# Optimization experiments

Measured on AMD Instinct MI355X. Metric: run time of the kernel, lower is better.

## Reference

```python
import jax, jax.numpy as jnp
import numpy as np

B, C, H, W = 4, 512, 96, 96
NH = 8
HD = C // NH
NC = 128
D = 768
L = H * W
EPS = 1e-5  # torch LayerNorm default


def _l2n(x, axis):
    # F.normalize: x / max(||x||, 1e-12)
    return x / jnp.maximum(jnp.linalg.norm(x, axis=axis, keepdims=True), 1e-12)


def _ln2d(x, g, b):
    # LayerNorm2d: normalize over channel dim of (B,C,H,W)
    mu = x.mean(1, keepdims=True)
    var = ((x - mu) ** 2).mean(1, keepdims=True)
    return (x - mu) / jnp.sqrt(var + EPS) * g[None, :, None, None] + b[None, :, None, None]


def _conv1x1(x, w):
    return jnp.einsum('oc,bchw->bohw', w, x)


def setup_inputs() -> dict:
    key = jax.random.key(0)
    ks = jax.random.split(key, 9)
    s = 0.02
    return {
        'img_feats': jax.random.normal(ks[0], (B, C, H, W), jnp.float32),
        'cls_embs': jax.random.normal(ks[1], (NC, D), jnp.float32),
        'cls_logits': jax.random.normal(ks[2], (B, NC), jnp.float32),
        'seg_logits': jax.random.normal(ks[3], (B, 1, H, W), jnp.float32),
        'gamma_g': jnp.ones((D,), jnp.float32), 'beta_g': jnp.zeros((D,), jnp.float32),
        'gamma_f': jnp.ones((C,), jnp.float32), 'beta_f': jnp.zeros((C,), jnp.float32),
        'attn_scale': jnp.ones((NH, 1, 1), jnp.float32),
        'Wg': jax.random.normal(ks[4], (C, D), jnp.float32) * s,
        'Wqkv': jax.random.normal(ks[5], (3 * C, C), jnp.float32) * s,
        'Wo': jax.random.normal(ks[6], (C, C), jnp.float32) * s,
        'bo': jnp.zeros((C,), jnp.float32),
        'gamma_n': jnp.ones((C,), jnp.float32), 'beta_n': jnp.zeros((C,), jnp.float32),
        'W1': jax.random.normal(ks[7], (C, C), jnp.float32) * s, 'b1': jnp.zeros((C,), jnp.float32),
        'W2': jax.random.normal(ks[8], (C, C), jnp.float32) * s, 'b2': jnp.zeros((C,), jnp.float32),
    }


def reference(img_feats, cls_embs, cls_logits, seg_logits, gamma_g, beta_g,
              gamma_f, beta_f, attn_scale, Wg, Wqkv, Wo, bo, gamma_n, beta_n,
              W1, b1, W2, b2):
    xn = _ln2d(img_feats, gamma_f, beta_f)
    # guide LayerNorm over embedding dim
    mu = cls_embs.mean(-1, keepdims=True)
    var = ((cls_embs - mu) ** 2).mean(-1, keepdims=True)
    cn = (cls_embs - mu) / jnp.sqrt(var + EPS) * gamma_g + beta_g
    g = (cn @ Wg.T).reshape(NC, NH, HD)  # nc nh hd

    qkv = _conv1x1(xn, Wqkv).reshape(B, 3, NH, HD, L)
    q, k, v = qkv[:, 0], qkv[:, 1], qkv[:, 2]  # each (B,NH,HD,L)

    # cosine guide map + min-max normalization + softmax-weighted aggregation over classes
    gm = jnp.einsum('nhd,bhdl->bhnl', _l2n(g, -1), _l2n(q, -2))
    gm = gm - gm.min(-1, keepdims=True)
    gm = gm / gm.max(-1, keepdims=True)
    gm = (jax.nn.softmax(gm, axis=2) * gm).sum(2, keepdims=True)  # (B,NH,1,L)

    # auxiliary guide map from cls logits + masked pooling of k
    cls_obj = jnp.einsum('nhd,bn->bhd', g, cls_logits)
    mask = jax.nn.sigmoid(seg_logits)  # (B,1,H,W)
    seg_obj = (mask * k.reshape(B, C, H, W)).sum((2, 3)) / mask.sum((2, 3))  # (B,C)
    obj = _l2n(cls_obj + seg_obj.reshape(B, NH, HD), -1)
    aux = jnp.einsum('bhd,bhdl->bhl', obj, _l2n(k, -2))[:, :, None, :]
    aux = aux - aux.min(-1, keepdims=True)
    aux = aux / aux.max(-1, keepdims=True)
    gm = gm * aux

    v = gm * v
    # channel (transposed) cosine attention: (B,NH,HD,HD)
    attn = jnp.einsum('bhdl,bhel->bhde', _l2n(q, -1), _l2n(k, -1)) * attn_scale
    out = jnp.einsum('bhde,bhel->bhdl', jax.nn.softmax(attn, -1), v).reshape(B, C, H, W)

    x = img_feats + _conv1x1(out, Wo) + bo[None, :, None, None]
    # ConvMlp with pre-norm: LayerNorm2d -> 1x1 conv -> GELU -> 1x1 conv
    fin = _ln2d(x, gamma_n, beta_n)
    h = jax.nn.gelu(_conv1x1(fin, W1) + b1[None, :, None, None], approximate=False)
    return x + _conv1x1(h, W2) + b2[None, :, None, None]
```

## Files before the change

kernel.cpp:

```cpp
#include <hip/hip_runtime.h>
#include <hip/hip_bf16.h>
#include <math.h>

#define BB 4
#define CC 512
#define NHEAD 8
#define HDIM 64
#define NCLS 128
#define DD 768
#define LL 9216
#define BLPIX 36864
#define EPSV 1e-5f
#define GMBLK 144
#define AUXBLK 36
#define LSPLIT 8
#define NLT 72

typedef __hip_bfloat16 bf16;
typedef __attribute__((ext_vector_type(8))) short short8v;
typedef __attribute__((ext_vector_type(4))) short short4v;
typedef __attribute__((ext_vector_type(4))) float f32x4;

__device__ __forceinline__ float bf2f(bf16 v){ return __bfloat162float(v); }
__device__ __forceinline__ bf16 f2bf(float v){ return __float2bfloat16(v); }
__device__ __forceinline__ short bfbits(float v){ bf16 b = __float2bfloat16(v); return *reinterpret_cast<short*>(&b); }
__device__ __forceinline__ float s2f(short s){ bf16 b = *reinterpret_cast<bf16*>(&s); return __bfloat162float(b); }

__global__ __launch_bounds__(256) void fuse_ln_k(const float* __restrict__ X,
    const float* __restrict__ lng, const float* __restrict__ lnb,
    bf16* __restrict__ xnT){
  __shared__ float sred[2][4][64];
  __shared__ float muS[64], rsS[64];
  __shared__ float t[64][65];
  int p0 = blockIdx.x * 64;
  int b = p0 / LL, l0 = p0 - b * LL;
  int tid = threadIdx.x;
  int cg = tid >> 6, l = tid & 63;
  const float* base = X + (size_t)b * CC * LL + l0 + l;
  float s = 0.f, ss = 0.f;
  for (int c = cg * 128; c < cg * 128 + 128; c++){
    float v = base[(size_t)c * LL];
    s += v; ss += v * v;
  }
  sred[0][cg][l] = s; sred[1][cg][l] = ss;
  __syncthreads();
  if (tid < 64){
    float st = sred[0][0][tid] + sred[0][1][tid] + sred[0][2][tid] + sred[0][3][tid];
    float sst = sred[1][0][tid] + sred[1][1][tid] + sred[1][2][tid] + sred[1][3][tid];
    float m = st * (1.0f / CC);
    float var = sst * (1.0f / CC) - m * m;
    muS[tid] = m; rsS[tid] = rsqrtf(var + EPSV);
  }
  __syncthreads();
  int pr = tid >> 4;
  int cc = (tid & 15) * 4;
  for (int cb = 0; cb < 8; cb++){
    int c0 = cb * 64;
    #pragma unroll
    for (int i = 0; i < 16; i++){
      int idx = i * 256 + tid;
      int cl = idx >> 6, ll2 = idx & 63;
      t[cl][ll2] = X[(size_t)b * CC * LL + (size_t)(c0 + cl) * LL + l0 + ll2];
    }
    __syncthreads();
    #pragma unroll
    for (int i = 0; i < 4; i++){
      int pl = pr + i * 16;
      int p = p0 + pl;
      float m = muS[pl], r = rsS[pl];
      short4v pk;
      #pragma unroll
      for (int e = 0; e < 4; e++){
        int c = c0 + cc + e;
        pk[e] = bfbits((t[cc + e][pl] - m) * r * lng[c] + lnb[c]);
      }
      *(short4v*)&xnT[(size_t)p * CC + c0 + cc] = pk;
    }
    __syncthreads();
  }
}

__global__ void wcast_k(const float* __restrict__ wqkv, const float* __restrict__ wo,
                        const float* __restrict__ w1, const float* __restrict__ w2,
                        bf16* __restrict__ oq, bf16* __restrict__ oo,
                        bf16* __restrict__ o1, bf16* __restrict__ o2){
  int i = blockIdx.x * 256 + threadIdx.x;
  int e = i * 4;
  const float* src; bf16* dst; int off;
  if (e < 786432){ src = wqkv; dst = oq; off = e; }
  else if (e < 1048576){ src = wo; dst = oo; off = e - 786432; }
  else if (e < 1310720){ src = w1; dst = o1; off = e - 1048576; }
  else { src = w2; dst = o2; off = e - 1310720; }
  float4 v = *reinterpret_cast<const float4*>(src + off);
  short4v pk;
  pk[0] = bfbits(v.x); pk[1] = bfbits(v.y); pk[2] = bfbits(v.z); pk[3] = bfbits(v.w);
  *(short4v*)&dst[off] = pk;
}

__global__ void statsred_k(const float2* __restrict__ statp, float* __restrict__ mu, float* __restrict__ rs){
  int p = blockIdx.x * 256 + threadIdx.x;
  if (p >= BLPIX) return;
  float s = 0.f, ss = 0.f;
  #pragma unroll
  for (int part = 0; part < 4; part++){
    float2 v = statp[part * BLPIX + p];
    s += v.x; ss += v.y;
  }
  float m = s * (1.0f / CC);
  float var = ss * (1.0f / CC) - m * m;
  mu[p] = m; rs[p] = rsqrtf(var + EPSV);
}

__global__ void rownorm_red_k(const float* __restrict__ qssp, const float* __restrict__ kssp,
                              float* __restrict__ qn, float* __restrict__ kn){
  int row = blockIdx.x;
  const float* src = (row < 2048) ? qssp : kssp;
  int r = (row < 2048) ? row : row - 2048;
  float s = 0.f;
  for (int i = threadIdx.x; i < NLT; i += 64) s += src[(size_t)r * NLT + i];
  #pragma unroll
  for (int m = 1; m < 64; m <<= 1) s += __shfl_xor(s, m);
  if (threadIdx.x == 0){
    float nv = fmaxf(sqrtf(s), 1e-12f);
    if (row < 2048) qn[r] = nv; else kn[r] = nv;
  }
}

template<int MODE>
__global__ __launch_bounds__(256, 2) void mgemm_k(
    const bf16* __restrict__ A,
    const bf16* __restrict__ B,
    const float* __restrict__ residf,
    const bf16* __restrict__ residb,
    const float* __restrict__ bias,
    const float* __restrict__ mu, const float* __restrict__ rs,
    const float* __restrict__ lng, const float* __restrict__ lnb,
    float2* __restrict__ statp,
    float* __restrict__ qssp, float* __restrict__ kssp,
    bf16* __restrict__ qo, bf16* __restrict__ ko, bf16* __restrict__ vo,
    bf16* __restrict__ xT_out,
    float* __restrict__ xo,
    bf16* __restrict__ ho)
{
  __shared__ short Asm[128 * 64];
  __shared__ short Bsm[128 * 64];
  __shared__ float sredf[512];
  int tid = threadIdx.x;
  int lane = tid & 63, wv = tid >> 6;
  int wr = wv >> 1, wc = wv & 1;
  int r15 = lane & 15, g = lane >> 4, h7 = lane & 7;
  int gx = gridDim.x;
  int flat = blockIdx.y * gx + blockIdx.x;
  int cpx = (gx * gridDim.y) >> 3;
  int swz = (flat & 7) * cpx + (flat >> 3);
  int m0 = (swz % gx) * 128, n0 = (swz / gx) * 128;
  int srow = tid >> 3, skkg = tid & 7;
  int sslot = ((skkg ^ (srow & 7))) * 8;

  f32x4 acc[4][4];
  #pragma unroll
  for (int i = 0; i < 4; i++)
    #pragma unroll
    for (int j = 0; j < 4; j++) acc[i][j] = (f32x4){0.f, 0.f, 0.f, 0.f};

  short8v pa[4], pb[4];
  auto loadAB = [&](int it){
    int k0 = it * 64;
    if (MODE == 2){
      int c0 = k0 + skkg * 8;
      float ga[8], be[8];
      *(float4*)&ga[0] = *(const float4*)&lng[c0];
      *(float4*)&ga[4] = *(const float4*)&lng[c0 + 4];
      *(float4*)&be[0] = *(const float4*)&lnb[c0];
      *(float4*)&be[4] = *(const float4*)&lnb[c0 + 4];
      #pragma unroll
      for (int r = 0; r < 4; r++){
        pa[r] = *reinterpret_cast<const short8v*>(A + (size_t)(m0 + r * 32 + srow) * 512 + c0);
        int rp = n0 + r * 32 + srow;
        float mm = mu[rp], rr = rs[rp];
        short8v raw = *reinterpret_cast<const short8v*>(B + (size_t)rp * 512 + c0);
        short8v ov;
        #pragma unroll
        for (int e = 0; e < 8; e++){
          float v = (s2f(raw[e]) - mm) * rr * ga[e] + be[e];
          ov[e] = bfbits(v);
        }
        pb[r] = ov;
      }
    } else {
      #pragma unroll
      for (int r = 0; r < 4; r++){
        pa[r] = *reinterpret_cast<const short8v*>(A + (size_t)(m0 + r * 32 + srow) * 512 + k0 + skkg * 8);
        pb[r] = *reinterpret_cast<const short8v*>(B + (size_t)(n0 + r * 32 + srow) * 512 + k0 + skkg * 8);
      }
    }
  };

  loadAB(0);
  for (int it = 0; it < 8; ++it){
    __syncthreads();
    #pragma unroll
    for (int r = 0; r < 4; r++){
      int row = r * 32 + srow;
      *(short8v*)&Asm[row * 64 + sslot] = pa[r];
      *(short8v*)&Bsm[row * 64 + sslot] = pb[r];
    }
    __syncthreads();
    if (it < 7) loadAB(it + 1);
    #pragma unroll
    for (int s = 0; s < 2; s++){
      int slot = ((s * 4 + g) ^ h7) * 8;
      short8v af[4], bf_[4];
      #pragma unroll
      for (int i = 0; i < 4; i++){
        af[i]  = *(const short8v*)&Asm[(wr * 64 + i * 16 + r15) * 64 + slot];
        bf_[i] = *(const short8v*)&Bsm[(wc * 64 + i * 16 + r15) * 64 + slot];
      }
      #pragma unroll
      for (int i = 0; i < 4; i++)
        #pragma unroll
        for (int j = 0; j < 4; j++){
          if (MODE == 2)
            acc[i][j] = __builtin_amdgcn_mfma_f32_16x16x32_bf16(bf_[i], af[j], acc[i][j], 0, 0, 0);
          else
            acc[i][j] = __builtin_amdgcn_mfma_f32_16x16x32_bf16(af[i], bf_[j], acc[i][j], 0, 0, 0);
        }
    }
  }

  int bIdx = n0 / LL;
  int lbase = n0 - bIdx * LL;
  if (MODE == 0){
    int part = m0 >> 9;
    if (part < 2){
      bf16* dst = (part == 0) ? qo : ko;
      int chb = (m0 & 511) + wr * 64;
      #pragma unroll
      for (int i = 0; i < 4; i++)
        #pragma unroll
        for (int j = 0; j < 4; j++){
          int l = lbase + wc * 64 + j * 16 + r15;
          #pragma unroll
          for (int e = 0; e < 4; e++){
            int ch = chb + i * 16 + g * 4 + e;
            dst[(size_t)bIdx * CC * LL + (size_t)ch * LL + l] = f2bf(acc[i][j][e]);
          }
        }
      #pragma unroll
      for (int i = 0; i < 4; i++)
        #pragma unroll
        for (int e = 0; e < 4; e++){
          float ssv = acc[i][0][e]*acc[i][0][e] + acc[i][1][e]*acc[i][1][e]
                    + acc[i][2][e]*acc[i][2][e] + acc[i][3][e]*acc[i][3][e];
          #pragma unroll
          for (int msk = 1; msk < 16; msk <<= 1) ssv += __shfl_xor(ssv, msk);
          if (r15 == 0) sredf[wv * 64 + i * 16 + g * 4 + e] = ssv;
        }
      __syncthreads();
      if (tid < 128){
        int wrr = tid >> 6, chL = tid & 63;
        float tot = sredf[(wrr * 2) * 64 + chL] + sredf[(wrr * 2 + 1) * 64 + chL];
        int c = (m0 & 511) + wrr * 64 + chL;
        int row = bIdx * 512 + c;
        int ltile = lbase >> 7;
        float* dd = (part == 0) ? qssp : kssp;
        dd[(size_t)row * NLT + ltile] = tot;
      }
    } else {
      int chb = (m0 & 511) + wr * 64;
      #pragma unroll
      for (int i = 0; i < 4; i++)
        #pragma unroll
        for (int j = 0; j < 4; j++){
          int l = lbase + wc * 64 + j * 16 + r15;
          int ch = chb + i * 16 + g * 4;
          short4v pk;
          #pragma unroll
          for (int e = 0; e < 4; e++) pk[e] = bfbits(acc[i][j][e]);
          *(short4v*)&vo[((size_t)bIdx * LL + l) * CC + ch] = pk;
        }
    }
  } else if (MODE == 1){
    float sj[4] = {0.f,0.f,0.f,0.f}, ssj[4] = {0.f,0.f,0.f,0.f};
    #pragma unroll
    for (int i = 0; i < 4; i++)
      #pragma unroll
      for (int j = 0; j < 4; j++){
        int l = lbase + wc * 64 + j * 16 + r15;
        int chm = m0 + wr * 64 + i * 16 + g * 4;
        short4v pk;
        #pragma unroll
        for (int e = 0; e < 4; e++){
          int m = chm + e;
          size_t o = (size_t)bIdx * CC * LL + (size_t)m * LL + l;
          float xv = residf[o] + acc[i][j][e] + bias[m];
          pk[e] = bfbits(xv);
          sj[j] += xv; ssj[j] += xv * xv;
        }
        *(short4v*)&xT_out[((size_t)bIdx * LL + l) * CC + chm] = pk;
      }
    #pragma unroll
    for (int j = 0; j < 4; j++){
      sj[j] += __shfl_xor(sj[j], 16); sj[j] += __shfl_xor(sj[j], 32);
      ssj[j] += __shfl_xor(ssj[j], 16); ssj[j] += __shfl_xor(ssj[j], 32);
    }
    if (g == 0){
      #pragma unroll
      for (int j = 0; j < 4; j++){
        sredf[wv * 128 + j * 32 + r15 * 2 + 0] = sj[j];
        sredf[wv * 128 + j * 32 + r15 * 2 + 1] = ssj[j];
      }
    }
    __syncthreads();
    if (tid < 128){
      int wv2 = tid >> 6, lane2 = tid & 63, j2 = lane2 >> 4, r2 = lane2 & 15;
      float s   = sredf[wv2 * 128 + j2 * 32 + r2 * 2 + 0] + sredf[(wv2 + 2) * 128 + j2 * 32 + r2 * 2 + 0];
      float ss2 = sredf[wv2 * 128 + j2 * 32 + r2 * 2 + 1] + sredf[(wv2 + 2) * 128 + j2 * 32 + r2 * 2 + 1];
      int p = n0 + wv2 * 64 + j2 * 16 + r2;
      statp[(m0 >> 7) * BLPIX + p] = make_float2(s, ss2);
    }
  } else if (MODE == 3){
    #pragma unroll
    for (int i = 0; i < 4; i++)
      #pragma unroll
      for (int j = 0; j < 4; j++){
        int l = lbase + wc * 64 + j * 16 + r15;
        int chm = m0 + wr * 64 + i * 16 + g * 4;
        short4v rv = *(const short4v*)&residb[((size_t)bIdx * LL + l) * CC + chm];
        #pragma unroll
        for (int e = 0; e < 4; e++){
          int m = chm + e;
          size_t o = (size_t)bIdx * CC * LL + (size_t)m * LL + l;
          xo[o] = s2f(rv[e]) + acc[i][j][e] + bias[m];
        }
      }
  } else {
    #pragma unroll
    for (int i = 0; i < 4; i++)
      #pragma unroll
      for (int j = 0; j < 4; j++){
        int mm = m0 + wr * 64 + j * 16 + r15;
        float bv = bias[mm];
        #pragma unroll
        for (int e = 0; e < 4; e++){
          int n = n0 + wc * 64 + i * 16 + g * 4 + e;
          float t = acc[i][j][e] + bv;
          float gv = 0.5f * t * (1.0f + erff(t * 0.70710678118654752f));
          ho[(size_t)n * CC + mm] = f2bf(gv);
        }
      }
  }
}

__global__ void clsg_k(const float* __restrict__ cls_embs, const float* __restrict__ gamma_g,
                       const float* __restrict__ beta_g, const float* __restrict__ Wg,
                       float* __restrict__ g, bf16* __restrict__ gnb){
  __shared__ float cn[DD];
  __shared__ float red[256];
  __shared__ float gsh[CC];
  __shared__ float nrm[NHEAD];
  int n = blockIdx.x;
  const float* e = cls_embs + (size_t)n * DD;
  float s = 0.f, ss = 0.f;
  for (int i = threadIdx.x; i < DD; i += 256){ float v = e[i]; s += v; ss += v * v; }
  red[threadIdx.x] = s; __syncthreads();
  for (int st = 128; st > 0; st >>= 1){ if (threadIdx.x < st) red[threadIdx.x] += red[threadIdx.x + st]; __syncthreads(); }
  float mean = red[0] / DD; __syncthreads();
  red[threadIdx.x] = ss; __syncthreads();
  for (int st = 128; st > 0; st >>= 1){ if (threadIdx.x < st) red[threadIdx.x] += red[threadIdx.x + st]; __syncthreads(); }
  float var = red[0] / DD - mean * mean;
  float rstd = rsqrtf(var + EPSV);
  __syncthreads();
  for (int i = threadIdx.x; i < DD; i += 256) cn[i] = (e[i] - mean) * rstd * gamma_g[i] + beta_g[i];
  __syncthreads();
  for (int c = threadIdx.x; c < CC; c += 256){
    const float* w = Wg + (size_t)c * DD;
    float a = 0.f;
    #pragma unroll 8
    for (int d = 0; d < DD; d++) a += cn[d] * w[d];
    gsh[c] = a;
  }
  __syncthreads();
  if (threadIdx.x < NHEAD){
    float a = 0.f;
    for (int d = 0; d < HDIM; d++){ float v = gsh[threadIdx.x * HDIM + d]; a += v * v; }
    nrm[threadIdx.x] = fmaxf(sqrtf(a), 1e-12f);
  }
  __syncthreads();
  for (int c = threadIdx.x; c < CC; c += 256){
    g[(size_t)n * CC + c] = gsh[c];
    gnb[(size_t)n * CC + c] = f2bf(gsh[c] / nrm[c >> 6]);
  }
}

__global__ void clsobj_k(const float* __restrict__ g, const float* __restrict__ cls_l,
                         float* __restrict__ cls_obj){
  int idx = blockIdx.x * 256 + threadIdx.x;
  if (idx >= BB * CC) return;
  int b = idx >> 9, c = idx & 511;
  float a = 0.f;
  for (int n = 0; n < NCLS; n++) a += g[(size_t)n * CC + c] * cls_l[b * NCLS + n];
  cls_obj[idx] = a;
}

__global__ __launch_bounds__(256) void gm1_k(const bf16* __restrict__ q, const bf16* __restrict__ gnb,
        float* __restrict__ pmin, float* __restrict__ pmax){
  __shared__ bf16 qs[64 * 68];
  __shared__ float sspart[4][64];
  __shared__ float rq[64];
  int bh = blockIdx.x, lt = blockIdx.y;
  int l0 = lt * 64;
  int t = threadIdx.x;
  int b = bh >> 3, h = bh & 7;
  int w = t >> 6, lane = t & 63, r15 = lane & 15, g = lane >> 4;
  const bf16* qp = q + (size_t)b * CC * LL + (size_t)h * HDIM * LL + l0;
  #pragma unroll
  for (int i2 = 0; i2 < 4; i2++){
    int idx = t + i2 * 256;
    int d = idx >> 4, lch = (idx & 15) * 4;
    short4v vv = *reinterpret_cast<const short4v*>(qp + (size_t)d * LL + lch);
    *(short4v*)&qs[d * 68 + lch] = vv;
  }
  __syncthreads();
  {
    int l = t & 63, dg = t >> 6;
    float ss = 0.f;
    #pragma unroll
    for (int dd = 0; dd < 16; dd++){ float v = bf2f(qs[(dg * 16 + dd) * 68 + l]); ss += v * v; }
    sspart[dg][l] = ss;
  }
  __syncthreads();
  if (t < 64){
    float ss = sspart[0][t] + sspart[1][t] + sspart[2][t] + sspart[3][t];
    rq[t] = 1.0f / fmaxf(sqrtf(ss), 1e-12f);
  }
  __syncthreads();
  short8v ag[2][2];
  #pragma unroll
  for (int i = 0; i < 2; i++)
    #pragma unroll
    for (int kt = 0; kt < 2; kt++)
      ag[i][kt] = *reinterpret_cast<const short8v*>(gnb + (size_t)(w * 32 + i * 16 + r15) * CC + h * 64 + kt * 32 + g * 8);
  short8v bq[4][2];
  #pragma unroll
  for (int j = 0; j < 4; j++){
    float rqv = rq[j * 16 + r15];
    #pragma unroll
    for (int kt = 0; kt < 2; kt++){
      short8v bb;
      #pragma unroll
      for (int jj = 0; jj < 8; jj++){
        int d = kt * 32 + g * 8 + jj;
        bb[jj] = bfbits(bf2f(qs[d * 68 + j * 16 + r15]) * rqv);
      }
      bq[j][kt] = bb;
    }
  }
  f32x4 acc[2][4];
  #pragma unroll
  for (int i = 0; i < 2; i++)
    #pragma unroll
    for (int j = 0; j < 4; j++) acc[i][j] = (f32x4){0.f,0.f,0.f,0.f};
  #pragma unroll
  for (int kt = 0; kt < 2; kt++)
    #pragma unroll
    for (int i = 0; i < 2; i++)
      #pragma unroll
      for (int j = 0; j < 4; j++)
        acc[i][j] = __builtin_amdgcn_mfma_f32_16x16x32_bf16(ag[i][kt], bq[j][kt], acc[i][j], 0, 0, 0);
  #pragma unroll
  for (int i = 0; i < 2; i++)
    #pragma unroll
    for (int e = 0; e < 4; e++){
      float mn = acc[i][0][e], mx = acc[i][0][e];
      #pragma unroll
      for (int j = 1; j < 4; j++){ mn = fminf(mn, acc[i][j][e]); mx = fmaxf(mx, acc[i][j][e]); }
      #pragma unroll
      for (int msk = 1; msk < 16; msk <<= 1){
        mn = fminf(mn, __shfl_xor(mn, msk));
        mx = fmaxf(mx, __shfl_xor(mx, msk));
      }
      if (r15 == 0){
        int n = w * 32 + i * 16 + g * 4 + e;
        pmin[((size_t)bh * 128 + n) * GMBLK + lt] = mn;
        pmax[((size_t)bh * 128 + n) * GMBLK + lt] = mx;
      }
    }
}

__global__ void gmred_k(const float* __restrict__ pmin, const float* __restrict__ pmax,
                        float* __restrict__ gmin, float* __restrict__ gms){
  __shared__ float rmn[64], rmx[64];
  int row = blockIdx.x;
  float mn = 1e30f, mx = -1e30f;
  for (int i = threadIdx.x; i < GMBLK; i += 64){
    mn = fminf(mn, pmin[(size_t)row * GMBLK + i]);
    mx = fmaxf(mx, pmax[(size_t)row * GMBLK + i]);
  }
  rmn[threadIdx.x] = mn; rmx[threadIdx.x] = mx; __syncthreads();
  for (int st = 32; st > 0; st >>= 1){
    if (threadIdx.x < st){
      rmn[threadIdx.x] = fminf(rmn[threadIdx.x], rmn[threadIdx.x + st]);
      rmx[threadIdx.x] = fmaxf(rmx[threadIdx.x], rmx[threadIdx.x + st]);
    }
    __syncthreads();
  }
  if (threadIdx.x == 0){ gmin[row] = rmn[0]; gms[row] = rmx[0] - rmn[0]; }
}

__global__ void seg_k(const float* __restrict__ seg, const bf16* __restrict__ k, float* __restrict__ seg_num){
  __shared__ float red[256];
  int bc = blockIdx.x;
  int b = bc >> 9;
  const bf16* p = k + (size_t)bc * LL;
  const float* sp = seg + (size_t)b * LL;
  float s = 0.f;
  for (int i = threadIdx.x; i < LL; i += 256){
    float m = 1.0f / (1.0f + expf(-sp[i]));
    s += m * bf2f(p[i]);
  }
  red[threadIdx.x] = s; __syncthreads();
  for (int st = 128; st > 0; st >>= 1){ if (threadIdx.x < st) red[threadIdx.x] += red[threadIdx.x + st]; __syncthreads(); }
  if (threadIdx.x == 0) seg_num[bc] = red[0];
}

__global__ void segden_k(const float* __restrict__ seg, float* __restrict__ den){
  __shared__ float red[256];
  int b = blockIdx.x;
  const float* sp = seg + (size_t)b * LL;
  float s = 0.f;
  for (int i = threadIdx.x; i < LL; i += 256) s += 1.0f / (1.0f + expf(-sp[i]));
  red[threadIdx.x] = s; __syncthreads();
  for (int st = 128; st > 0; st >>= 1){ if (threadIdx.x < st) red[threadIdx.x] += red[threadIdx.x + st]; __syncthreads(); }
  if (threadIdx.x == 0) den[b] = red[0];
}

__global__ void obj_k(const float* __restrict__ cls_obj, const float* __restrict__ seg_num,
                      const float* __restrict__ den, float* __restrict__ obj){
  __shared__ float sval[2048];
  __shared__ float nrm[32];
  int tid = threadIdx.x;
  #pragma unroll
  for (int i = 0; i < 8; i++){
    int idx = tid + i * 256;
    int b = idx >> 9;
    sval[idx] = cls_obj[idx] + seg_num[idx] / den[b];
  }
  __syncthreads();
  if (tid < 32){
    float s = 0.f;
    for (int d = 0; d < 64; d++){ float v = sval[tid * 64 + d]; s += v * v; }
    nrm[tid] = fmaxf(sqrtf(s), 1e-12f);
  }
  __syncthreads();
  #pragma unroll
  for (int i = 0; i < 8; i++){
    int idx = tid + i * 256;
    obj[idx] = sval[idx] / nrm[idx >> 6];
  }
}

__global__ void aux_k(const bf16* __restrict__ k, const float* __restrict__ obj, float* __restrict__ aux,
                      float* __restrict__ pmin, float* __restrict__ pmax){
  __shared__ float os[64];
  __shared__ float rmn[256], rmx[256];
  int bh = blockIdx.x, lt = blockIdx.y;
  int b = bh >> 3, h = bh & 7;
  int l = lt * 256 + threadIdx.x;
  if (threadIdx.x < 64) os[threadIdx.x] = obj[bh * 64 + threadIdx.x];
  __syncthreads();
  const bf16* kp = k + (size_t)b * CC * LL + (size_t)h * HDIM * LL + l;
  float ss = 0.f, dot = 0.f;
  #pragma unroll 8
  for (int d = 0; d < 64; d++){ float v = bf2f(kp[(size_t)d * LL]); ss += v * v; dot += os[d] * v; }
  float av = dot / fmaxf(sqrtf(ss), 1e-12f);
  aux[(size_t)bh * LL + l] = av;
  rmn[threadIdx.x] = av; rmx[threadIdx.x] = av; __syncthreads();
  for (int st = 128; st > 0; st >>= 1){
    if (threadIdx.x < st){
      rmn[threadIdx.x] = fminf(rmn[threadIdx.x], rmn[threadIdx.x + st]);
      rmx[threadIdx.x] = fmaxf(rmx[threadIdx.x], rmx[threadIdx.x + st]);
    }
    __syncthreads();
  }
  if (threadIdx.x == 0){ pmin[bh * AUXBLK + lt] = rmn[0]; pmax[bh * AUXBLK + lt] = rmx[0]; }
}

__global__ void auxred_k(const float* __restrict__ pmin, const float* __restrict__ pmax,
                         float* __restrict__ amin, float* __restrict__ ams){
  __shared__ float rmn[64], rmx[64];
  int bh = blockIdx.x;
  float mn = 1e30f, mx = -1e30f;
  for (int i = threadIdx.x; i < AUXBLK; i += 64){
    mn = fminf(mn, pmin[bh * AUXBLK + i]);
    mx = fmaxf(mx, pmax[bh * AUXBLK + i]);
  }
  rmn[threadIdx.x] = mn; rmx[threadIdx.x] = mx; __syncthreads();
  for (int st = 32; st > 0; st >>= 1){
    if (threadIdx.x < st){
      rmn[threadIdx.x] = fminf(rmn[threadIdx.x], rmn[threadIdx.x + st]);
      rmx[threadIdx.x] = fmaxf(rmx[threadIdx.x], rmx[threadIdx.x + st]);
    }
    __syncthreads();
  }
  if (threadIdx.x == 0){ amin[bh] = rmn[0]; ams[bh] = rmx[0] - rmn[0]; }
}

__global__ __launch_bounds__(256) void attn_k(const bf16* __restrict__ q, const bf16* __restrict__ k,
                                              float* __restrict__ part){
  __shared__ float red[4 * 4096];
  int ls = blockIdx.x, bh = blockIdx.y;
  int b = bh >> 3, h = bh & 7;
  int t = threadIdx.x;
  int w = t >> 6, lane = t & 63, r15 = lane & 15, g = lane >> 4;
  const bf16* qp = q + (size_t)b * CC * LL + (size_t)h * HDIM * LL;
  const bf16* kp = k + (size_t)b * CC * LL + (size_t)h * HDIM * LL;
  int kbase = ls * 1152 + w * 288;
  f32x4 acc[4][4];
  #pragma unroll
  for (int i = 0; i < 4; i++)
    #pragma unroll
    for (int j = 0; j < 4; j++) acc[i][j] = (f32x4){0.f,0.f,0.f,0.f};
  for (int ks = 0; ks < 9; ks++){
    int koff = kbase + ks * 32 + g * 8;
    short8v aq[4], bk[4];
    #pragma unroll
    for (int i = 0; i < 4; i++) aq[i] = *reinterpret_cast<const short8v*>(qp + (size_t)(i * 16 + r15) * LL + koff);
    #pragma unroll
    for (int j = 0; j < 4; j++) bk[j] = *reinterpret_cast<const short8v*>(kp + (size_t)(j * 16 + r15) * LL + koff);
    #pragma unroll
    for (int i = 0; i < 4; i++)
      #pragma unroll
      for (int j = 0; j < 4; j++)
        acc[i][j] = __builtin_amdgcn_mfma_f32_16x16x32_bf16(aq[i], bk[j], acc[i][j], 0, 0, 0);
  }
  #pragma unroll
  for (int i = 0; i < 4; i++)
    #pragma unroll
    for (int j = 0; j < 4; j++)
      #pragma unroll
      for (int e = 0; e < 4; e++)
        red[w * 4096 + (i * 16 + g * 4 + e) * 64 + j * 16 + r15] = acc[i][j][e];
  __syncthreads();
  #pragma unroll
  for (int it = 0; it < 16; it++){
    int idx = t + it * 256;
    part[((size_t)(bh * LSPLIT + ls)) * 4096 + idx] = red[idx] + red[4096 + idx] + red[8192 + idx] + red[12288 + idx];
  }
}

__global__ void smax_k(const float* __restrict__ part, const float* __restrict__ qn,
                       const float* __restrict__ kn, const float* __restrict__ scale,
                       bf16* __restrict__ Pb){
  __shared__ float As[64 * 65];
  int bh = blockIdx.x;
  int h = bh & 7;
  int tid = threadIdx.x;
  #pragma unroll
  for (int i = 0; i < 16; i++){
    int cell = tid + i * 256;
    int d = cell >> 6, e = cell & 63;
    float s = 0.f;
    #pragma unroll
    for (int ls = 0; ls < LSPLIT; ls++) s += part[((size_t)(bh * LSPLIT + ls)) * 4096 + cell];
    As[d * 65 + e] = s * scale[h] / (qn[bh * 64 + d] * kn[bh * 64 + e]);
  }
  __syncthreads();
  if (tid < 64){
    int d = tid;
    float mx = -1e30f;
    for (int e = 0; e < 64; e++) mx = fmaxf(mx, As[d * 65 + e]);
    float sum = 0.f;
    for (int e = 0; e < 64; e++){ float ev = expf(As[d * 65 + e] - mx); As[d * 65 + e] = ev; sum += ev; }
    float inv = 1.0f / sum;
    for (int e = 0; e < 64; e++) Pb[(size_t)bh * 4096 + d * 64 + e] = f2bf(As[d * 65 + e] * inv);
  }
}

__global__ __launch_bounds__(256) void pv_k(const bf16* __restrict__ q, const bf16* __restrict__ gnb,
      const float* __restrict__ aux,
      const float* __restrict__ gmin, const float* __restrict__ gms,
      const float* __restrict__ amin, const float* __restrict__ ams,
      const bf16* __restrict__ Pb, const bf16* __restrict__ vT, bf16* __restrict__ outT){
  __shared__ bf16 qs[64 * 68];
  __shared__ float sspart[4][64];
  __shared__ float rq[64];
  __shared__ float gminS[128], rgmsS[128];
  __shared__ float separt[4][64], setpart[4][64];
  __shared__ float wl[64];
  int bh = blockIdx.x, lt = blockIdx.y;
  int l0 = lt * 64;
  int t = threadIdx.x;
  int b = bh >> 3, h = bh & 7;
  int w = t >> 6, lane = t & 63, r15 = lane & 15, g = lane >> 4;
  if (t < 128){ gminS[t] = gmin[bh * 128 + t]; rgmsS[t] = 1.0f / gms[bh * 128 + t]; }
  const bf16* qp = q + (size_t)b * CC * LL + (size_t)h * HDIM * LL + l0;
  #pragma unroll
  for (int i2 = 0; i2 < 4; i2++){
    int idx = t + i2 * 256;
    int d = idx >> 4, lch = (idx & 15) * 4;
    short4v vv = *reinterpret_cast<const short4v*>(qp + (size_t)d * LL + lch);
    *(short4v*)&qs[d * 68 + lch] = vv;
  }
  __syncthreads();
  {
    int l = t & 63, dg = t >> 6;
    float ss = 0.f;
    #pragma unroll
    for (int dd = 0; dd < 16; dd++){ float v = bf2f(qs[(dg * 16 + dd) * 68 + l]); ss += v * v; }
    sspart[dg][l] = ss;
  }
  __syncthreads();
  if (t < 64){
    float ss = sspart[0][t] + sspart[1][t] + sspart[2][t] + sspart[3][t];
    rq[t] = 1.0f / fmaxf(sqrtf(ss), 1e-12f);
  }
  __syncthreads();
  short8v ag[2][2];
  #pragma unroll
  for (int i = 0; i < 2; i++)
    #pragma unroll
    for (int kt = 0; kt < 2; kt++)
      ag[i][kt] = *reinterpret_cast<const short8v*>(gnb + (size_t)(w * 32 + i * 16 + r15) * CC + h * 64 + kt * 32 + g * 8);
  short8v bq[4][2];
  #pragma unroll
  for (int j = 0; j < 4; j++){
    float rqv = rq[j * 16 + r15];
    #pragma unroll
    for (int kt = 0; kt < 2; kt++){
      short8v bb;
      #pragma unroll
      for (int jj = 0; jj < 8; jj++){
        int d = kt * 32 + g * 8 + jj;
        bb[jj] = bfbits(bf2f(qs[d * 68 + j * 16 + r15]) * rqv);
      }
      bq[j][kt] = bb;
    }
  }
  f32x4 acc[2][4];
  #pragma unroll
  for (int i = 0; i < 2; i++)
    #pragma unroll
    for (int j = 0; j < 4; j++) acc[i][j] = (f32x4){0.f,0.f,0.f,0.f};
  #pragma unroll
  for (int kt = 0; kt < 2; kt++)
    #pragma unroll
    for (int i = 0; i < 2; i++)
      #pragma unroll
      for (int j = 0; j < 4; j++)
        acc[i][j] = __builtin_amdgcn_mfma_f32_16x16x32_bf16(ag[i][kt], bq[j][kt], acc[i][j], 0, 0, 0);
  float seL[4] = {0.f,0.f,0.f,0.f}, setL[4] = {0.f,0.f,0.f,0.f};
  #pragma unroll
  for (int i = 0; i < 2; i++)
    #pragma unroll
    for (int j = 0; j < 4; j++)
      #pragma unroll
      for (int e = 0; e < 4; e++){
        int n = w * 32 + i * 16 + g * 4 + e;
        float tt = (acc[i][j][e] - gminS[n]) * rgmsS[n];
        float ee = __expf(tt);
        seL[j] += ee; setL[j] += ee * tt;
      }
  #pragma unroll
  for (int j = 0; j < 4; j++){
    seL[j] += __shfl_xor(seL[j], 16); seL[j] += __shfl_xor(seL[j], 32);
    setL[j] += __shfl_xor(setL[j], 16); setL[j] += __shfl_xor(setL[j], 32);
  }
  if (g == 0){
    #pragma unroll
    for (int j = 0; j < 4; j++){ separt[w][j * 16 + r15] = seL[j]; setpart[w][j * 16 + r15] = setL[j]; }
  }
  __syncthreads();
  if (t < 64){
    float se = separt[0][t] + separt[1][t] + separt[2][t] + separt[3][t];
    float st = setpart[0][t] + setpart[1][t] + setpart[2][t] + setpart[3][t];
    float gmred = st / se;
    float auxn = (aux[(size_t)bh * LL + l0 + t] - amin[bh]) / ams[bh];
    wl[t] = gmred * auxn;
  }
  __syncthreads();
  short8v ap[4][2];
  #pragma unroll
  for (int i = 0; i < 4; i++)
    #pragma unroll
    for (int kt = 0; kt < 2; kt++)
      ap[i][kt] = *reinterpret_cast<const short8v*>(Pb + (size_t)bh * 4096 + (i * 16 + r15) * 64 + kt * 32 + g * 8);
  const bf16* vrow = vT + ((size_t)b * LL + l0 + w * 16 + r15) * CC + h * 64;
  short8v bv[2];
  #pragma unroll
  for (int kt = 0; kt < 2; kt++) bv[kt] = *reinterpret_cast<const short8v*>(vrow + kt * 32 + g * 8);
  f32x4 oacc[4];
  #pragma unroll
  for (int i = 0; i < 4; i++) oacc[i] = (f32x4){0.f,0.f,0.f,0.f};
  #pragma unroll
  for (int kt = 0; kt < 2; kt++)
    #pragma unroll
    for (int i = 0; i < 4; i++)
      oacc[i] = __builtin_amdgcn_mfma_f32_16x16x32_bf16(ap[i][kt], bv[kt], oacc[i], 0, 0, 0);
  float wlv = wl[w * 16 + r15];
  bf16* orow = outT + ((size_t)b * LL + l0 + w * 16 + r15) * CC + h * 64;
  #pragma unroll
  for (int i = 0; i < 4; i++){
    short4v pk;
    #pragma unroll
    for (int e = 0; e < 4; e++) pk[e] = bfbits(oacc[i][e] * wlv);
    *(short4v*)&orow[i * 16 + g * 4] = pk;
  }
}

extern "C" void kernel_launch(void* const* d_in, const int* in_sizes, int n_in,
                              void* d_out, int out_size, void* d_ws, size_t ws_size,
                              hipStream_t stream){
  const float* img        = (const float*)d_in[0];
  const float* cls_embs   = (const float*)d_in[1];
  const float* cls_logits = (const float*)d_in[2];
  const float* seg        = (const float*)d_in[3];
  const float* gamma_g    = (const float*)d_in[4];
  const float* beta_g     = (const float*)d_in[5];
  const float* gamma_f    = (const float*)d_in[6];
  const float* beta_f     = (const float*)d_in[7];
  const float* attn_scale = (const float*)d_in[8];
  const float* Wg         = (const float*)d_in[9];
  const float* Wqkv       = (const float*)d_in[10];
  const float* Wo         = (const float*)d_in[11];
  const float* bo         = (const float*)d_in[12];
  const float* gamma_n    = (const float*)d_in[13];
  const float* beta_n     = (const float*)d_in[14];
  const float* W1         = (const float*)d_in[15];
  const float* b1         = (const float*)d_in[16];
  const float* W2         = (const float*)d_in[17];
  const float* b2         = (const float*)d_in[18];
  float* outp = (float*)d_out;
  (void)in_sizes; (void)n_in; (void)out_size;

  char* wsb = (char*)d_ws;
  size_t off = 0;
  auto alloc = [&](size_t bytes)->char*{
    char* p = wsb + off;
    off += (bytes + 255) & ~(size_t)255;
    return p;
  };
  float* mu1   = (float*)alloc((size_t)BLPIX * 4);
  float* rs1   = (float*)alloc((size_t)BLPIX * 4);
  float2* statp= (float2*)alloc((size_t)4 * BLPIX * 8);
  float* qssp  = (float*)alloc((size_t)2048 * NLT * 4);
  float* kssp  = (float*)alloc((size_t)2048 * NLT * 4);
  float* qn    = (float*)alloc(2048 * 4);
  float* kn    = (float*)alloc(2048 * 4);
  float* gbuf  = (float*)alloc((size_t)NCLS * CC * 4);
  bf16*  gnbb  = (bf16*)alloc((size_t)NCLS * CC * 2);
  float* clsov = (float*)alloc(2048 * 4);
  float* segn  = (float*)alloc(2048 * 4);
  float* segd  = (float*)alloc(256);
  float* objv  = (float*)alloc(2048 * 4);
  float* gminp = (float*)alloc((size_t)32 * 128 * GMBLK * 4);
  float* gmaxp = (float*)alloc((size_t)32 * 128 * GMBLK * 4);
  float* gminv = (float*)alloc(4096 * 4);
  float* gmsv  = (float*)alloc(4096 * 4);
  float* auxv  = (float*)alloc((size_t)32 * LL * 4);
  float* apmin = (float*)alloc(32 * AUXBLK * 4);
  float* apmax = (float*)alloc(32 * AUXBLK * 4);
  float* aminv = (float*)alloc(256);
  float* amsv  = (float*)alloc(256);
  bf16*  Pb    = (bf16*)alloc((size_t)32 * 4096 * 2);
  float* apart = (float*)alloc((size_t)32 * LSPLIT * 4096 * 4);
  bf16* qb    = (bf16*)alloc((size_t)BB * CC * LL * 2);
  bf16* kb    = (bf16*)alloc((size_t)BB * CC * LL * 2);
  bf16* wqkvb = (bf16*)alloc((size_t)1536 * 512 * 2);
  bf16* wob   = (bf16*)alloc((size_t)512 * 512 * 2);
  bf16* w1b   = (bf16*)alloc((size_t)512 * 512 * 2);
  bf16* w2b   = (bf16*)alloc((size_t)512 * 512 * 2);
  bf16* vT  = (bf16*)d_out;
  bf16* xnT = (bf16*)((char*)d_out + (size_t)BB * CC * LL * 2);
  bf16* outT = kb;
  bf16* xT   = qb;
  bf16* hbT  = kb;
  if (off > ws_size) return;

  wcast_k<<<1536, 256, 0, stream>>>(Wqkv, Wo, W1, W2, wqkvb, wob, w1b, w2b);
  fuse_ln_k<<<576, 256, 0, stream>>>(img, gamma_f, beta_f, xnT);
  mgemm_k<0><<<dim3(12, 288), 256, 0, stream>>>(wqkvb, xnT, nullptr, nullptr, nullptr,
      nullptr, nullptr, nullptr, nullptr, nullptr, qssp, kssp,
      qb, kb, vT, nullptr, nullptr, nullptr);
  rownorm_red_k<<<4096, 64, 0, stream>>>(qssp, kssp, qn, kn);
  clsg_k<<<NCLS, 256, 0, stream>>>(cls_embs, gamma_g, beta_g, Wg, gbuf, gnbb);
  clsobj_k<<<8, 256, 0, stream>>>(gbuf, cls_logits, clsov);
  gm1_k<<<dim3(32, GMBLK), 256, 0, stream>>>(qb, gnbb, gminp, gmaxp);
  gmred_k<<<4096, 64, 0, stream>>>(gminp, gmaxp, gminv, gmsv);
  seg_k<<<2048, 256, 0, stream>>>(seg, kb, segn);
  segden_k<<<BB, 256, 0, stream>>>(seg, segd);
  obj_k<<<1, 256, 0, stream>>>(clsov, segn, segd, objv);
  aux_k<<<dim3(32, AUXBLK), 256, 0, stream>>>(kb, objv, auxv, apmin, apmax);
  auxred_k<<<32, 64, 0, stream>>>(apmin, apmax, aminv, amsv);
  attn_k<<<dim3(LSPLIT, 32), 256, 0, stream>>>(qb, kb, apart);
  smax_k<<<32, 256, 0, stream>>>(apart, qn, kn, attn_scale, Pb);
  pv_k<<<dim3(32, GMBLK), 256, 0, stream>>>(qb, gnbb, auxv, gminv, gmsv, aminv, amsv, Pb, vT, outT);
  mgemm_k<1><<<dim3(4, 288), 256, 0, stream>>>(wob, outT, img, nullptr, bo,
      nullptr, nullptr, nullptr, nullptr, statp, nullptr, nullptr,
      nullptr, nullptr, nullptr, xT, nullptr, nullptr);
  statsred_k<<<BLPIX / 256, 256, 0, stream>>>(statp, mu1, rs1);
  mgemm_k<2><<<dim3(4, 288), 256, 0, stream>>>(w1b, xT, nullptr, nullptr, b1,
      mu1, rs1, gamma_n, beta_n, nullptr, nullptr, nullptr,
      nullptr, nullptr, nullptr, nullptr, nullptr, hbT);
  mgemm_k<3><<<dim3(4, 288), 256, 0, stream>>>(w2b, hbT, nullptr, xT, b2,
      nullptr, nullptr, nullptr, nullptr, nullptr, nullptr, nullptr,
      nullptr, nullptr, nullptr, nullptr, outp, nullptr);
}
```

Measured before the change: 463.8 us.

## Merge independent small kernels into multi-role mega-kernels to cut launch count

Combines the weight cast, input LayerNorm transpose and class-guide projection into one launch. It also merges the guide-map partial min/max, the Q·K^T channel attention, the segmentation pooling and the row-norm reduction into one multi-role kernel, and folds the class-object matmul into extra blocks of the QKV GEMM. The three reduction kernels become a single launch as well. The aim is to remove launch overhead and tail idle time from many small serial kernels. In exchange the attention partial now uses fewer warps per block with longer K loops, and the guide-map kernel recomputes q norms inside the kernel.

Result: slower. 476.8 us (+2.8%).

```diff
diff --git a/kernel.cpp b/kernel.cpp
--- a/kernel.cpp
+++ b/kernel.cpp
@@ -26,75 +26,124 @@
 __device__ __forceinline__ short bfbits(float v){ bf16 b = __float2bfloat16(v); return *reinterpret_cast<short*>(&b); }
 __device__ __forceinline__ float s2f(short s){ bf16 b = *reinterpret_cast<bf16*>(&s); return __bfloat162float(b); }
 
-__global__ __launch_bounds__(256) void fuse_ln_k(const float* __restrict__ X,
-    const float* __restrict__ lng, const float* __restrict__ lnb,
-    bf16* __restrict__ xnT){
-  __shared__ float sred[2][4][64];
-  __shared__ float muS[64], rsS[64];
-  __shared__ float t[64][65];
-  int p0 = blockIdx.x * 64;
-  int b = p0 / LL, l0 = p0 - b * LL;
+__global__ __launch_bounds__(256) void mega0_k(
+    const float* __restrict__ wqkv, const float* __restrict__ wo,
+    const float* __restrict__ w1, const float* __restrict__ w2,
+    bf16* __restrict__ oq, bf16* __restrict__ oo,
+    bf16* __restrict__ o1, bf16* __restrict__ o2,
+    const float* __restrict__ X, const float* __restrict__ lng, const float* __restrict__ lnb,
+    bf16* __restrict__ xnT,
+    const float* __restrict__ cls_embs, const float* __restrict__ gamma_g,
+    const float* __restrict__ beta_g, const float* __restrict__ Wg,
+    float* __restrict__ g, bf16* __restrict__ gnb)
+{
+  __shared__ __align__(16) char raw[19200];
+  int bid = blockIdx.x;
   int tid = threadIdx.x;
-  int cg = tid >> 6, l = tid & 63;
-  const float* base = X + (size_t)b * CC * LL + l0 + l;
-  float s = 0.f, ss = 0.f;
-  for (int c = cg * 128; c < cg * 128 + 128; c++){
-    float v = base[(size_t)c * LL];
-    s += v; ss += v * v;
-  }
-  sred[0][cg][l] = s; sred[1][cg][l] = ss;
-  __syncthreads();
-  if (tid < 64){
-    float st = sred[0][0][tid] + sred[0][1][tid] + sred[0][2][tid] + sred[0][3][tid];
-    float sst = sred[1][0][tid] + sred[1][1][tid] + sred[1][2][tid] + sred[1][3][tid];
-    float m = st * (1.0f / CC);
-    float var = sst * (1.0f / CC) - m * m;
-    muS[tid] = m; rsS[tid] = rsqrtf(var + EPSV);
-  }
-  __syncthreads();
-  int pr = tid >> 4;
-  int cc = (tid & 15) * 4;
-  for (int cb = 0; cb < 8; cb++){
-    int c0 = cb * 64;
-    #pragma unroll
-    for (int i = 0; i < 16; i++){
-      int idx = i * 256 + tid;
-      int cl = idx >> 6, ll2 = idx & 63;
-      t[cl][ll2] = X[(size_t)b * CC * LL + (size_t)(c0 + cl) * LL + l0 + ll2];
-    }
-    __syncthreads();
-    #pragma unroll
-    for (int i = 0; i < 4; i++){
-      int pl = pr + i * 16;
-      int p = p0 + pl;
-      float m = muS[pl], r = rsS[pl];
-      short4v pk;
-      #pragma unroll
-      for (int e = 0; e < 4; e++){
-        int c = c0 + cc + e;
-        pk[e] = bfbits((t[cc + e][pl] - m) * r * lng[c] + lnb[c]);
-      }
-      *(short4v*)&xnT[(size_t)p * CC + c0 + cc] = pk;
-    }
-    __syncthreads();
-  }
-}
-
-__global__ void wcast_k(const float* __restrict__ wqkv, const float* __restrict__ wo,
-                        const float* __restrict__ w1, const float* __restrict__ w2,
-                        bf16* __restrict__ oq, bf16* __restrict__ oo,
-                        bf16* __restrict__ o1, bf16* __restrict__ o2){
-  int i = blockIdx.x * 256 + threadIdx.x;
-  int e = i * 4;
-  const float* src; bf16* dst; int off;
-  if (e < 786432){ src = wqkv; dst = oq; off = e; }
-  else if (e < 1048576){ src = wo; dst = oo; off = e - 786432; }
-  else if (e < 1310720){ src = w1; dst = o1; off = e - 1048576; }
-  else { src = w2; dst = o2; off = e - 1310720; }
-  float4 v = *reinterpret_cast<const float4*>(src + off);
-  short4v pk;
-  pk[0] = bfbits(v.x); pk[1] = bfbits(v.y); pk[2] = bfbits(v.z); pk[3] = bfbits(v.w);
-  *(short4v*)&dst[off] = pk;
+  if (bid < 1536){
+    int i = bid * 256 + tid;
+    int e = i * 4;
+    const float* src; bf16* dst; int off;
+    if (e < 786432){ src = wqkv; dst = oq; off = e; }
+    else if (e < 1048576){ src = wo; dst = oo; off = e - 786432; }
+    else if (e < 1310720){ src = w1; dst = o1; off = e - 1048576; }
+    else { src = w2; dst = o2; off = e - 1310720; }
+    float4 v = *reinterpret_cast<const float4*>(src + off);
+    short4v pk;
+    pk[0] = bfbits(v.x); pk[1] = bfbits(v.y); pk[2] = bfbits(v.z); pk[3] = bfbits(v.w);
+    *(short4v*)&dst[off] = pk;
+    return;
+  }
+  if (bid < 2112){
+    float* sred = (float*)raw;
+    float* muS  = (float*)(raw + 2048);
+    float* rsS  = (float*)(raw + 2304);
+    float (*t)[65] = (float(*)[65])(raw + 2560);
+    int p0 = (bid - 1536) * 64;
+    int b = p0 / LL, l0 = p0 - b * LL;
+    int cg = tid >> 6, l = tid & 63;
+    const float* base = X + (size_t)b * CC * LL + l0 + l;
+    float s = 0.f, ss = 0.f;
+    for (int c = cg * 128; c < cg * 128 + 128; c++){
+      float v = base[(size_t)c * LL];
+      s += v; ss += v * v;
+    }
+    sred[0 * 256 + cg * 64 + l] = s; sred[1 * 256 + cg * 64 + l] = ss;
+    __syncthreads();
+    if (tid < 64){
+      float st = sred[tid] + sred[64 + tid] + sred[128 + tid] + sred[192 + tid];
+      float sst = sred[256 + tid] + sred[320 + tid] + sred[384 + tid] + sred[448 + tid];
+      float m = st * (1.0f / CC);
+      float var = sst * (1.0f / CC) - m * m;
+      muS[tid] = m; rsS[tid] = rsqrtf(var + EPSV);
+    }
+    __syncthreads();
+    int pr = tid >> 4;
+    int cc = (tid & 15) * 4;
+    for (int cb = 0; cb < 8; cb++){
+      int c0 = cb * 64;
+      #pragma unroll
+      for (int i = 0; i < 16; i++){
+        int idx = i * 256 + tid;
+        int cl = idx >> 6, ll2 = idx & 63;
+        t[cl][ll2] = X[(size_t)b * CC * LL + (size_t)(c0 + cl) * LL + l0 + ll2];
+      }
+      __syncthreads();
+      #pragma unroll
+      for (int i = 0; i < 4; i++){
+        int pl = pr + i * 16;
+        int p = p0 + pl;
+        float m = muS[pl], r = rsS[pl];
+        short4v pk;
+        #pragma unroll
+        for (int e = 0; e < 4; e++){
+          int c = c0 + cc + e;
+          pk[e] = bfbits((t[cc + e][pl] - m) * r * lng[c] + lnb[c]);
+        }
+        *(short4v*)&xnT[(size_t)p * CC + c0 + cc] = pk;
+      }
+      __syncthreads();
+    }
+    return;
+  }
+  {
+    float* cn  = (float*)raw;
+    float* red = (float*)(raw + 3072);
+    float* gsh = (float*)(raw + 4096);
+    float* nrm = (float*)(raw + 6144);
+    int n = bid - 2112;
+    const float* e = cls_embs + (size_t)n * DD;
+    float s = 0.f, ss = 0.f;
+    for (int i = tid; i < DD; i += 256){ float v = e[i]; s += v; ss += v * v; }
+    red[tid] = s; __syncthreads();
+    for (int st = 128; st > 0; st >>= 1){ if (tid < st) red[tid] += red[tid + st]; __syncthreads(); }
+    float mean = red[0] / DD; __syncthreads();
+    red[tid] = ss; __syncthreads();
+    for (int st = 128; st > 0; st >>= 1){ if (tid < st) red[tid] += red[tid + st]; __syncthreads(); }
+    float var = red[0] / DD - mean * mean;
+    float rstd = rsqrtf(var + EPSV);
+    __syncthreads();
+    for (int i = tid; i < DD; i += 256) cn[i] = (e[i] - mean) * rstd * gamma_g[i] + beta_g[i];
+    __syncthreads();
+    for (int c = tid; c < CC; c += 256){
+      const float* w = Wg + (size_t)c * DD;
+      float a = 0.f;
+      #pragma unroll 8
+      for (int d = 0; d < DD; d++) a += cn[d] * w[d];
+      gsh[c] = a;
+    }
+    __syncthreads();
+    if (tid < NHEAD){
+      float a = 0.f;
+      for (int d = 0; d < HDIM; d++){ float v = gsh[tid * HDIM + d]; a += v * v; }
+      nrm[tid] = fmaxf(sqrtf(a), 1e-12f);
+    }
+    __syncthreads();
+    for (int c = tid; c < CC; c += 256){
+      g[(size_t)n * CC + c] = gsh[c];
+      gnb[(size_t)n * CC + c] = f2bf(gsh[c] / nrm[c >> 6]);
+    }
+  }
 }
 
 __global__ void statsred_k(const float2* __restrict__ statp, float* __restrict__ mu, float* __restrict__ rs){
@@ -109,21 +158,6 @@
   float m = s * (1.0f / CC);
   float var = ss * (1.0f / CC) - m * m;
   mu[p] = m; rs[p] = rsqrtf(var + EPSV);
-}
-
-__global__ void rownorm_red_k(const float* __restrict__ qssp, const float* __restrict__ kssp,
-                              float* __restrict__ qn, float* __restrict__ kn){
-  int row = blockIdx.x;
-  const float* src = (row < 2048) ? qssp : kssp;
-  int r = (row < 2048) ? row : row - 2048;
-  float s = 0.f;
-  for (int i = threadIdx.x; i < NLT; i += 64) s += src[(size_t)r * NLT + i];
-  #pragma unroll
-  for (int m = 1; m < 64; m <<= 1) s += __shfl_xor(s, m);
-  if (threadIdx.x == 0){
-    float nv = fmaxf(sqrtf(s), 1e-12f);
-    if (row < 2048) qn[r] = nv; else kn[r] = nv;
-  }
 }
 
 template<int MODE>
@@ -140,18 +174,27 @@
     bf16* __restrict__ qo, bf16* __restrict__ ko, bf16* __restrict__ vo,
     bf16* __restrict__ xT_out,
     float* __restrict__ xo,
-    bf16* __restrict__ ho)
+    bf16* __restrict__ ho,
+    const float* __restrict__ gA, const float* __restrict__ clsl, float* __restrict__ clsovO)
 {
   __shared__ short Asm[128 * 64];
   __shared__ short Bsm[128 * 64];
   __shared__ float sredf[512];
   int tid = threadIdx.x;
+  if (MODE == 0 && blockIdx.x >= 3456){
+    int idx = (blockIdx.x - 3456) * 256 + tid;
+    int b = idx >> 9, c = idx & 511;
+    float a = 0.f;
+    for (int n = 0; n < NCLS; n++) a += gA[(size_t)n * CC + c] * clsl[b * NCLS + n];
+    clsovO[idx] = a;
+    return;
+  }
   int lane = tid & 63, wv = tid >> 6;
   int wr = wv >> 1, wc = wv & 1;
   int r15 = lane & 15, g = lane >> 4, h7 = lane & 7;
-  int gx = gridDim.x;
-  int flat = blockIdx.y * gx + blockIdx.x;
-  int cpx = (gx * gridDim.y) >> 3;
+  int flat, gx, cpx;
+  if (MODE == 0){ flat = blockIdx.x; gx = 12; cpx = 432; }
+  else { gx = gridDim.x; flat = blockIdx.y * gx + blockIdx.x; cpx = (gx * gridDim.y) >> 3; }
   int swz = (flat & 7) * cpx + (flat >> 3);
   int m0 = (swz % gx) * 128, n0 = (swz / gx) * 128;
   int srow = tid >> 3, skkg = tid & 7;
@@ -178,11 +221,11 @@
         pa[r] = *reinterpret_cast<const short8v*>(A + (size_t)(m0 + r * 32 + srow) * 512 + c0);
         int rp = n0 + r * 32 + srow;
         float mm = mu[rp], rr = rs[rp];
-        short8v raw = *reinterpret_cast<const short8v*>(B + (size_t)rp * 512 + c0);
+        short8v rawv = *reinterpret_cast<const short8v*>(B + (size_t)rp * 512 + c0);
         short8v ov;
         #pragma unroll
         for (int e = 0; e < 8; e++){
-          float v = (s2f(raw[e]) - mm) * rr * ga[e] + be[e];
+          float v = (s2f(rawv[e]) - mm) * rr * ga[e] + be[e];
           ov[e] = bfbits(v);
         }
         pb[r] = ov;
@@ -352,222 +395,190 @@
   }
 }
 
-__global__ void clsg_k(const float* __restrict__ cls_embs, const float* __restrict__ gamma_g,
-                       const float* __restrict__ beta_g, const float* __restrict__ Wg,
-                       float* __restrict__ g, bf16* __restrict__ gnb){
-  __shared__ float cn[DD];
-  __shared__ float red[256];
-  __shared__ float gsh[CC];
-  __shared__ float nrm[NHEAD];
-  int n = blockIdx.x;
-  const float* e = cls_embs + (size_t)n * DD;
-  float s = 0.f, ss = 0.f;
-  for (int i = threadIdx.x; i < DD; i += 256){ float v = e[i]; s += v; ss += v * v; }
-  red[threadIdx.x] = s; __syncthreads();
-  for (int st = 128; st > 0; st >>= 1){ if (threadIdx.x < st) red[threadIdx.x] += red[threadIdx.x + st]; __syncthreads(); }
-  float mean = red[0] / DD; __syncthreads();
-  red[threadIdx.x] = ss; __syncthreads();
-  for (int st = 128; st > 0; st >>= 1){ if (threadIdx.x < st) red[threadIdx.x] += red[threadIdx.x + st]; __syncthreads(); }
-  float var = red[0] / DD - mean * mean;
-  float rstd = rsqrtf(var + EPSV);
-  __syncthreads();
-  for (int i = threadIdx.x; i < DD; i += 256) cn[i] = (e[i] - mean) * rstd * gamma_g[i] + beta_g[i];
-  __syncthreads();
-  for (int c = threadIdx.x; c < CC; c += 256){
-    const float* w = Wg + (size_t)c * DD;
-    float a = 0.f;
-    #pragma unroll 8
-    for (int d = 0; d < DD; d++) a += cn[d] * w[d];
-    gsh[c] = a;
-  }
-  __syncthreads();
-  if (threadIdx.x < NHEAD){
-    float a = 0.f;
-    for (int d = 0; d < HDIM; d++){ float v = gsh[threadIdx.x * HDIM + d]; a += v * v; }
-    nrm[threadIdx.x] = fmaxf(sqrtf(a), 1e-12f);
-  }
-  __syncthreads();
-  for (int c = threadIdx.x; c < CC; c += 256){
-    g[(size_t)n * CC + c] = gsh[c];
-    gnb[(size_t)n * CC + c] = f2bf(gsh[c] / nrm[c >> 6]);
+__global__ __launch_bounds__(256) void mega1_k(
+    const bf16* __restrict__ q, const bf16* __restrict__ k, const bf16* __restrict__ gnb,
+    float* __restrict__ pmin, float* __restrict__ pmax,
+    float* __restrict__ part,
+    const float* __restrict__ seg, float* __restrict__ seg_num, float* __restrict__ den,
+    const float* __restrict__ qssp, const float* __restrict__ kssp,
+    float* __restrict__ qn, float* __restrict__ kn)
+{
+  __shared__ __align__(16) char raw[9984];
+  int bid = blockIdx.x;
+  int t = threadIdx.x;
+  if (bid < 4608){
+    bf16* qs = (bf16*)raw;
+    float (*sspart)[64] = (float(*)[64])(raw + 8704);
+    float* rq = (float*)(raw + 8704 + 1024);
+    int bh = bid & 31, lt = bid >> 5;
+    int l0 = lt * 64;
+    int b = bh >> 3, h = bh & 7;
+    int w = t >> 6, lane = t & 63, r15 = lane & 15, g = lane >> 4;
+    const bf16* qp = q + (size_t)b * CC * LL + (size_t)h * HDIM * LL + l0;
+    #pragma unroll
+    for (int i2 = 0; i2 < 4; i2++){
+      int idx = t + i2 * 256;
+      int d = idx >> 4, lch = (idx & 15) * 4;
+      short4v vv = *reinterpret_cast<const short4v*>(qp + (size_t)d * LL + lch);
+      *(short4v*)&qs[d * 68 + lch] = vv;
+    }
+    __syncthreads();
+    {
+      int l = t & 63, dg = t >> 6;
+      float ss = 0.f;
+      #pragma unroll
+      for (int dd = 0; dd < 16; dd++){ float v = bf2f(qs[(dg * 16 + dd) * 68 + l]); ss += v * v; }
+      sspart[dg][l] = ss;
+    }
+    __syncthreads();
+    if (t < 64){
+      float ss = sspart[0][t] + sspart[1][t] + sspart[2][t] + sspart[3][t];
+      rq[t] = 1.0f / fmaxf(sqrtf(ss), 1e-12f);
+    }
+    __syncthreads();
+    short8v ag[2][2];
+    #pragma unroll
+    for (int i = 0; i < 2; i++)
+      #pragma unroll
+      for (int kt = 0; kt < 2; kt++)
+        ag[i][kt] = *reinterpret_cast<const short8v*>(gnb + (size_t)(w * 32 + i * 16 + r15) * CC + h * 64 + kt * 32 + g * 8);
+    short8v bq[4][2];
+    #pragma unroll
+    for (int j = 0; j < 4; j++){
+      float rqv = rq[j * 16 + r15];
+      #pragma unroll
+      for (int kt = 0; kt < 2; kt++){
+        short8v bb;
+        #pragma unroll
+        for (int jj = 0; jj < 8; jj++){
+          int d = kt * 32 + g * 8 + jj;
+          bb[jj] = bfbits(bf2f(qs[d * 68 + j * 16 + r15]) * rqv);
+        }
+        bq[j][kt] = bb;
+      }
+    }
+    f32x4 acc[2][4];
+    #pragma unroll
+    for (int i = 0; i < 2; i++)
+      #pragma unroll
+      for (int j = 0; j < 4; j++) acc[i][j] = (f32x4){0.f,0.f,0.f,0.f};
+    #pragma unroll
+    for (int kt = 0; kt < 2; kt++)
+      #pragma unroll
+      for (int i = 0; i < 2; i++)
+        #pragma unroll
+        for (int j = 0; j < 4; j++)
+          acc[i][j] = __builtin_amdgcn_mfma_f32_16x16x32_bf16(ag[i][kt], bq[j][kt], acc[i][j], 0, 0, 0);
+    #pragma unroll
+    for (int i = 0; i < 2; i++)
+      #pragma unroll
+      for (int e = 0; e < 4; e++){
+        float mn = acc[i][0][e], mx = acc[i][0][e];
+        #pragma unroll
+        for (int j = 1; j < 4; j++){ mn = fminf(mn, acc[i][j][e]); mx = fmaxf(mx, acc[i][j][e]); }
+        #pragma unroll
+        for (int msk = 1; msk < 16; msk <<= 1){
+          mn = fminf(mn, __shfl_xor(mn, msk));
+          mx = fmaxf(mx, __shfl_xor(mx, msk));
+        }
+        if (r15 == 0){
+          int n = w * 32 + i * 16 + g * 4 + e;
+          pmin[((size_t)bh * 128 + n) * GMBLK + lt] = mn;
+          pmax[((size_t)bh * 128 + n) * GMBLK + lt] = mx;
+        }
+      }
+    return;
+  }
+  if (bid < 4864){
+    int bid2 = bid - 4608;
+    int ls = bid2 & 7, bh = bid2 >> 3;
+    int b = bh >> 3, h = bh & 7;
+    int w = t >> 6, lane = t & 63, r15 = lane & 15, g = lane >> 4;
+    const bf16* qp = q + (size_t)b * CC * LL + (size_t)h * HDIM * LL;
+    const bf16* kp = k + (size_t)b * CC * LL + (size_t)h * HDIM * LL;
+    int kbase = ls * 1152;
+    f32x4 acc4[4];
+    #pragma unroll
+    for (int j = 0; j < 4; j++) acc4[j] = (f32x4){0.f,0.f,0.f,0.f};
+    for (int ks = 0; ks < 36; ks++){
+      int koff = kbase + ks * 32 + g * 8;
+      short8v aq = *reinterpret_cast<const short8v*>(qp + (size_t)(w * 16 + r15) * LL + koff);
+      short8v bk[4];
+      #pragma unroll
+      for (int j = 0; j < 4; j++) bk[j] = *reinterpret_cast<const short8v*>(kp + (size_t)(j * 16 + r15) * LL + koff);
+      #pragma unroll
+      for (int j = 0; j < 4; j++)
+        acc4[j] = __builtin_amdgcn_mfma_f32_16x16x32_bf16(aq, bk[j], acc4[j], 0, 0, 0);
+    }
+    #pragma unroll
+    for (int j = 0; j < 4; j++)
+      #pragma unroll
+      for (int e = 0; e < 4; e++){
+        int d = w * 16 + g * 4 + e;
+        int ee = j * 16 + r15;
+        part[((size_t)(bh * LSPLIT + ls)) * 4096 + d * 64 + ee] = acc4[j][e];
+      }
+    return;
+  }
+  if (bid < 6912){
+    float* red = (float*)raw;
+    int bc = bid - 4864;
+    int b = bc >> 9;
+    const bf16* p = k + (size_t)bc * LL;
+    const float* sp = seg + (size_t)b * LL;
+    float s = 0.f;
+    for (int i = t; i < LL; i += 256){
+      float m = 1.0f / (1.0f + expf(-sp[i]));
+      s += m * bf2f(p[i]);
+    }
+    red[t] = s; __syncthreads();
+    for (int st = 128; st > 0; st >>= 1){ if (t < st) red[t] += red[t + st]; __syncthreads(); }
+    if (t == 0) seg_num[bc] = red[0];
+    return;
+  }
+  if (bid < 6916){
+    float* red = (float*)raw;
+    int b = bid - 6912;
+    const float* sp = seg + (size_t)b * LL;
+    float s = 0.f;
+    for (int i = t; i < LL; i += 256) s += 1.0f / (1.0f + expf(-sp[i]));
+    red[t] = s; __syncthreads();
+    for (int st = 128; st > 0; st >>= 1){ if (t < st) red[t] += red[t + st]; __syncthreads(); }
+    if (t == 0) den[b] = red[0];
+    return;
+  }
+  {
+    int r4 = (bid - 6916) * 4 + (t >> 6);
+    int lane = t & 63;
+    const float* src = (r4 < 2048) ? qssp : kssp;
+    int r = r4 & 2047;
+    float s = src[(size_t)r * NLT + lane] + ((lane < 8) ? src[(size_t)r * NLT + 64 + lane] : 0.f);
+    #pragma unroll
+    for (int m = 1; m < 64; m <<= 1) s += __shfl_xor(s, m);
+    if (lane == 0){
+      float nv = fmaxf(sqrtf(s), 1e-12f);
+      if (r4 < 2048) qn[r] = nv; else kn[r] = nv;
+    }
   }
 }
 
-__global__ void clsobj_k(const float* __restrict__ g, const float* __restrict__ cls_l,
-                         float* __restrict__ cls_obj){
-  int idx = blockIdx.x * 256 + threadIdx.x;
-  if (idx >= BB * CC) return;
-  int b = idx >> 9, c = idx & 511;
-  float a = 0.f;
-  for (int n = 0; n < NCLS; n++) a += g[(size_t)n * CC + c] * cls_l[b * NCLS + n];
-  cls_obj[idx] = a;
-}
-
-__global__ __launch_bounds__(256) void gm1_k(const bf16* __restrict__ q, const bf16* __restrict__ gnb,
-        float* __restrict__ pmin, float* __restrict__ pmax){
-  __shared__ bf16 qs[64 * 68];
-  __shared__ float sspart[4][64];
-  __shared__ float rq[64];
-  int bh = blockIdx.x, lt = blockIdx.y;
-  int l0 = lt * 64;
-  int t = threadIdx.x;
-  int b = bh >> 3, h = bh & 7;
-  int w = t >> 6, lane = t & 63, r15 = lane & 15, g = lane >> 4;
-  const bf16* qp = q + (size_t)b * CC * LL + (size_t)h * HDIM * LL + l0;
-  #pragma unroll
-  for (int i2 = 0; i2 < 4; i2++){
-    int idx = t + i2 * 256;
-    int d = idx >> 4, lch = (idx & 15) * 4;
-    short4v vv = *reinterpret_cast<const short4v*>(qp + (size_t)d * LL + lch);
-    *(short4v*)&qs[d * 68 + lch] = vv;
-  }
-  __syncthreads();
-  {
-    int l = t & 63, dg = t >> 6;
-    float ss = 0.f;
-    #pragma unroll
-    for (int dd = 0; dd < 16; dd++){ float v = bf2f(qs[(dg * 16 + dd) * 68 + l]); ss += v * v; }
-    sspart[dg][l] = ss;
-  }
-  __syncthreads();
-  if (t < 64){
-    float ss = sspart[0][t] + sspart[1][t] + sspart[2][t] + sspart[3][t];
-    rq[t] = 1.0f / fmaxf(sqrtf(ss), 1e-12f);
-  }
-  __syncthreads();
-  short8v ag[2][2];
-  #pragma unroll
-  for (int i = 0; i < 2; i++)
-    #pragma unroll
-    for (int kt = 0; kt < 2; kt++)
-      ag[i][kt] = *reinterpret_cast<const short8v*>(gnb + (size_t)(w * 32 + i * 16 + r15) * CC + h * 64 + kt * 32 + g * 8);
-  short8v bq[4][2];
-  #pragma unroll
-  for (int j = 0; j < 4; j++){
-    float rqv = rq[j * 16 + r15];
-    #pragma unroll
-    for (int kt = 0; kt < 2; kt++){
-      short8v bb;
-      #pragma unroll
-      for (int jj = 0; jj < 8; jj++){
-        int d = kt * 32 + g * 8 + jj;
-        bb[jj] = bfbits(bf2f(qs[d * 68 + j * 16 + r15]) * rqv);
-      }
-      bq[j][kt] = bb;
-    }
-  }
-  f32x4 acc[2][4];
-  #pragma unroll
-  for (int i = 0; i < 2; i++)
-    #pragma unroll
-    for (int j = 0; j < 4; j++) acc[i][j] = (f32x4){0.f,0.f,0.f,0.f};
-  #pragma unroll
-  for (int kt = 0; kt < 2; kt++)
-    #pragma unroll
-    for (int i = 0; i < 2; i++)
-      #pragma unroll
-      for (int j = 0; j < 4; j++)
-        acc[i][j] = __builtin_amdgcn_mfma_f32_16x16x32_bf16(ag[i][kt], bq[j][kt], acc[i][j], 0, 0, 0);
-  #pragma unroll
-  for (int i = 0; i < 2; i++)
-    #pragma unroll
-    for (int e = 0; e < 4; e++){
-      float mn = acc[i][0][e], mx = acc[i][0][e];
-      #pragma unroll
-      for (int j = 1; j < 4; j++){ mn = fminf(mn, acc[i][j][e]); mx = fmaxf(mx, acc[i][j][e]); }
-      #pragma unroll
-      for (int msk = 1; msk < 16; msk <<= 1){
-        mn = fminf(mn, __shfl_xor(mn, msk));
-        mx = fmaxf(mx, __shfl_xor(mx, msk));
-      }
-      if (r15 == 0){
-        int n = w * 32 + i * 16 + g * 4 + e;
-        pmin[((size_t)bh * 128 + n) * GMBLK + lt] = mn;
-        pmax[((size_t)bh * 128 + n) * GMBLK + lt] = mx;
-      }
-    }
-}
-
-__global__ void gmred_k(const float* __restrict__ pmin, const float* __restrict__ pmax,
-                        float* __restrict__ gmin, float* __restrict__ gms){
-  __shared__ float rmn[64], rmx[64];
-  int row = blockIdx.x;
-  float mn = 1e30f, mx = -1e30f;
-  for (int i = threadIdx.x; i < GMBLK; i += 64){
-    mn = fminf(mn, pmin[(size_t)row * GMBLK + i]);
-    mx = fmaxf(mx, pmax[(size_t)row * GMBLK + i]);
-  }
-  rmn[threadIdx.x] = mn; rmx[threadIdx.x] = mx; __syncthreads();
-  for (int st = 32; st > 0; st >>= 1){
-    if (threadIdx.x < st){
-      rmn[threadIdx.x] = fminf(rmn[threadIdx.x], rmn[threadIdx.x + st]);
-      rmx[threadIdx.x] = fmaxf(rmx[threadIdx.x], rmx[threadIdx.x + st]);
-    }
-    __syncthreads();
-  }
-  if (threadIdx.x == 0){ gmin[row] = rmn[0]; gms[row] = rmx[0] - rmn[0]; }
-}
-
-__global__ void seg_k(const float* __restrict__ seg, const bf16* __restrict__ k, float* __restrict__ seg_num){
-  __shared__ float red[256];
-  int bc = blockIdx.x;
-  int b = bc >> 9;
-  const bf16* p = k + (size_t)bc * LL;
-  const float* sp = seg + (size_t)b * LL;
-  float s = 0.f;
-  for (int i = threadIdx.x; i < LL; i += 256){
-    float m = 1.0f / (1.0f + expf(-sp[i]));
-    s += m * bf2f(p[i]);
-  }
-  red[threadIdx.x] = s; __syncthreads();
-  for (int st = 128; st > 0; st >>= 1){ if (threadIdx.x < st) red[threadIdx.x] += red[threadIdx.x + st]; __syncthreads(); }
-  if (threadIdx.x == 0) seg_num[bc] = red[0];
-}
-
-__global__ void segden_k(const float* __restrict__ seg, float* __restrict__ den){
-  __shared__ float red[256];
-  int b = blockIdx.x;
-  const float* sp = seg + (size_t)b * LL;
-  float s = 0.f;
-  for (int i = threadIdx.x; i < LL; i += 256) s += 1.0f / (1.0f + expf(-sp[i]));
-  red[threadIdx.x] = s; __syncthreads();
-  for (int st = 128; st > 0; st >>= 1){ if (threadIdx.x < st) red[threadIdx.x] += red[threadIdx.x + st]; __syncthreads(); }
-  if (threadIdx.x == 0) den[b] = red[0];
-}
-
-__global__ void obj_k(const float* __restrict__ cls_obj, const float* __restrict__ seg_num,
-                      const float* __restrict__ den, float* __restrict__ obj){
-  __shared__ float sval[2048];
-  __shared__ float nrm[32];
-  int tid = threadIdx.x;
-  #pragma unroll
-  for (int i = 0; i < 8; i++){
-    int idx = tid + i * 256;
-    int b = idx >> 9;
-    sval[idx] = cls_obj[idx] + seg_num[idx] / den[b];
-  }
-  __syncthreads();
-  if (tid < 32){
-    float s = 0.f;
-    for (int d = 0; d < 64; d++){ float v = sval[tid * 64 + d]; s += v * v; }
-    nrm[tid] = fmaxf(sqrtf(s), 1e-12f);
-  }
-  __syncthreads();
-  #pragma unroll
-  for (int i = 0; i < 8; i++){
-    int idx = tid + i * 256;
-    obj[idx] = sval[idx] / nrm[idx >> 6];
-  }
-}
-
-__global__ void aux_k(const bf16* __restrict__ k, const float* __restrict__ obj, float* __restrict__ aux,
+__global__ void aux_k(const bf16* __restrict__ k,
+                      const float* __restrict__ clsov, const float* __restrict__ segn,
+                      const float* __restrict__ segd,
+                      float* __restrict__ aux,
                       float* __restrict__ pmin, float* __restrict__ pmax){
   __shared__ float os[64];
   __shared__ float rmn[256], rmx[256];
   int bh = blockIdx.x, lt = blockIdx.y;
   int b = bh >> 3, h = bh & 7;
   int l = lt * 256 + threadIdx.x;
-  if (threadIdx.x < 64) os[threadIdx.x] = obj[bh * 64 + threadIdx.x];
+  if (threadIdx.x < 64){
+    float sv = clsov[bh * 64 + threadIdx.x] + segn[bh * 64 + threadIdx.x] / segd[b];
+    float ss = sv * sv;
+    #pragma unroll
+    for (int m = 1; m < 64; m <<= 1) ss += __shfl_xor(ss, m);
+    os[threadIdx.x] = sv / fmaxf(sqrtf(ss), 1e-12f);
+  }
   __syncthreads();
   const bf16* kp = k + (size_t)b * CC * LL + (size_t)h * HDIM * LL + l;
   float ss = 0.f, dot = 0.f;
@@ -586,94 +597,72 @@
   if (threadIdx.x == 0){ pmin[bh * AUXBLK + lt] = rmn[0]; pmax[bh * AUXBLK + lt] = rmx[0]; }
 }
 
-__global__ void auxred_k(const float* __restrict__ pmin, const float* __restrict__ pmax,
-                         float* __restrict__ amin, float* __restrict__ ams){
-  __shared__ float rmn[64], rmx[64];
-  int bh = blockIdx.x;
-  float mn = 1e30f, mx = -1e30f;
-  for (int i = threadIdx.x; i < AUXBLK; i += 64){
-    mn = fminf(mn, pmin[bh * AUXBLK + i]);
-    mx = fmaxf(mx, pmax[bh * AUXBLK + i]);
-  }
-  rmn[threadIdx.x] = mn; rmx[threadIdx.x] = mx; __syncthreads();
-  for (int st = 32; st > 0; st >>= 1){
-    if (threadIdx.x < st){
-      rmn[threadIdx.x] = fminf(rmn[threadIdx.x], rmn[threadIdx.x + st]);
-      rmx[threadIdx.x] = fmaxf(rmx[threadIdx.x], rmx[threadIdx.x + st]);
-    }
-    __syncthreads();
-  }
-  if (threadIdx.x == 0){ amin[bh] = rmn[0]; ams[bh] = rmx[0] - rmn[0]; }
-}
-
-__global__ __launch_bounds__(256) void attn_k(const bf16* __restrict__ q, const bf16* __restrict__ k,
-                                              float* __restrict__ part){
-  __shared__ float red[4 * 4096];
-  int ls = blockIdx.x, bh = blockIdx.y;
-  int b = bh >> 3, h = bh & 7;
-  int t = threadIdx.x;
-  int w = t >> 6, lane = t & 63, r15 = lane & 15, g = lane >> 4;
-  const bf16* qp = q + (size_t)b * CC * LL + (size_t)h * HDIM * LL;
-  const bf16* kp = k + (size_t)b * CC * LL + (size_t)h * HDIM * LL;
-  int kbase = ls * 1152 + w * 288;
-  f32x4 acc[4][4];
-  #pragma unroll
-  for (int i = 0; i < 4; i++)
-    #pragma unroll
-    for (int j = 0; j < 4; j++) acc[i][j] = (f32x4){0.f,0.f,0.f,0.f};
-  for (int ks = 0; ks < 9; ks++){
-    int koff = kbase + ks * 32 + g * 8;
-    short8v aq[4], bk[4];
-    #pragma unroll
-    for (int i = 0; i < 4; i++) aq[i] = *reinterpret_cast<const short8v*>(qp + (size_t)(i * 16 + r15) * LL + koff);
-    #pragma unroll
-    for (int j = 0; j < 4; j++) bk[j] = *reinterpret_cast<const short8v*>(kp + (size_t)(j * 16 + r15) * LL + koff);
-    #pragma unroll
-    for (int i = 0; i < 4; i++)
-      #pragma unroll
-      for (int j = 0; j < 4; j++)
-        acc[i][j] = __builtin_amdgcn_mfma_f32_16x16x32_bf16(aq[i], bk[j], acc[i][j], 0, 0, 0);
-  }
-  #pragma unroll
-  for (int i = 0; i < 4; i++)
-    #pragma unroll
-    for (int j = 0; j < 4; j++)
-      #pragma unroll
-      for (int e = 0; e < 4; e++)
-        red[w * 4096 + (i * 16 + g * 4 + e) * 64 + j * 16 + r15] = acc[i][j][e];
-  __syncthreads();
-  #pragma unroll
-  for (int it = 0; it < 16; it++){
-    int idx = t + it * 256;
-    part[((size_t)(bh * LSPLIT + ls)) * 4096 + idx] = red[idx] + red[4096 + idx] + red[8192 + idx] + red[12288 + idx];
-  }
-}
-
-__global__ void smax_k(const float* __restrict__ part, const float* __restrict__ qn,
-                       const float* __restrict__ kn, const float* __restrict__ scale,
-                       bf16* __restrict__ Pb){
+__global__ __launch_bounds__(256) void megared_k(
+    const float* __restrict__ gpmin, const float* __restrict__ gpmax,
+    float* __restrict__ gmin, float* __restrict__ gms,
+    const float* __restrict__ apmin, const float* __restrict__ apmax,
+    float* __restrict__ amin, float* __restrict__ ams,
+    const float* __restrict__ part, const float* __restrict__ qn,
+    const float* __restrict__ kn, const float* __restrict__ scale,
+    bf16* __restrict__ Pb)
+{
   __shared__ float As[64 * 65];
-  int bh = blockIdx.x;
-  int h = bh & 7;
+  int bid = blockIdx.x;
   int tid = threadIdx.x;
-  #pragma unroll
-  for (int i = 0; i < 16; i++){
-    int cell = tid + i * 256;
-    int d = cell >> 6, e = cell & 63;
-    float s = 0.f;
-    #pragma unroll
-    for (int ls = 0; ls < LSPLIT; ls++) s += part[((size_t)(bh * LSPLIT + ls)) * 4096 + cell];
-    As[d * 65 + e] = s * scale[h] / (qn[bh * 64 + d] * kn[bh * 64 + e]);
-  }
-  __syncthreads();
-  if (tid < 64){
-    int d = tid;
-    float mx = -1e30f;
-    for (int e = 0; e < 64; e++) mx = fmaxf(mx, As[d * 65 + e]);
-    float sum = 0.f;
-    for (int e = 0; e < 64; e++){ float ev = expf(As[d * 65 + e] - mx); As[d * 65 + e] = ev; sum += ev; }
-    float inv = 1.0f / sum;
-    for (int e = 0; e < 64; e++) Pb[(size_t)bh * 4096 + d * 64 + e] = f2bf(As[d * 65 + e] * inv);
+  if (bid < 1024){
+    int row = bid * 4 + (tid >> 6);
+    int lane = tid & 63;
+    float mn = gpmin[(size_t)row * GMBLK + lane];
+    float mx = gpmax[(size_t)row * GMBLK + lane];
+    mn = fminf(mn, gpmin[(size_t)row * GMBLK + 64 + lane]);
+    mx = fmaxf(mx, gpmax[(size_t)row * GMBLK + 64 + lane]);
+    if (lane < 16){
+      mn = fminf(mn, gpmin[(size_t)row * GMBLK + 128 + lane]);
+      mx = fmaxf(mx, gpmax[(size_t)row * GMBLK + 128 + lane]);
+    }
+    #pragma unroll
+    for (int m = 1; m < 64; m <<= 1){
+      mn = fminf(mn, __shfl_xor(mn, m));
+      mx = fmaxf(mx, __shfl_xor(mx, m));
+    }
+    if (lane == 0){ gmin[row] = mn; gms[row] = mx - mn; }
+    return;
+  }
+  if (bid < 1032){
+    int bh = (bid - 1024) * 4 + (tid >> 6);
+    int lane = tid & 63;
+    float mn = (lane < AUXBLK) ? apmin[bh * AUXBLK + lane] : 1e30f;
+    float mx = (lane < AUXBLK) ? apmax[bh * AUXBLK + lane] : -1e30f;
+    #pragma unroll
+    for (int m = 1; m < 64; m <<= 1){
+      mn = fminf(mn, __shfl_xor(mn, m));
+      mx = fmaxf(mx, __shfl_xor(mx, m));
+    }
+    if (lane == 0){ amin[bh] = mn; ams[bh] = mx - mn; }
+    return;
+  }
+  {
+    int bh = bid - 1032;
+    int h = bh & 7;
+    #pragma unroll
+    for (int i = 0; i < 16; i++){
+      int cell = tid + i * 256;
+      int d = cell >> 6, e = cell & 63;
+      float s = 0.f;
+      #pragma unroll
+      for (int ls = 0; ls < LSPLIT; ls++) s += part[((size_t)(bh * LSPLIT + ls)) * 4096 + cell];
+      As[d * 65 + e] = s * scale[h] / (qn[bh * 64 + d] * kn[bh * 64 + e]);
+    }
+    __syncthreads();
+    if (tid < 64){
+      int d = tid;
+      float mx = -1e30f;
+      for (int e = 0; e < 64; e++) mx = fmaxf(mx, As[d * 65 + e]);
+      float sum = 0.f;
+      for (int e = 0; e < 64; e++){ float ev = expf(As[d * 65 + e] - mx); As[d * 65 + e] = ev; sum += ev; }
+      float inv = 1.0f / sum;
+      for (int e = 0; e < 64; e++) Pb[(size_t)bh * 4096 + d * 64 + e] = f2bf(As[d * 65 + e] * inv);
+    }
   }
 }
 
@@ -852,7 +841,6 @@
   float* clsov = (float*)alloc(2048 * 4);
   float* segn  = (float*)alloc(2048 * 4);
   float* segd  = (float*)alloc(256);
-  float* objv  = (float*)alloc(2048 * 4);
   float* gminp = (float*)alloc((size_t)32 * 128 * GMBLK * 4);
   float* gmaxp = (float*)alloc((size_t)32 * 128 * GMBLK * 4);
   float* gminv = (float*)alloc(4096 * 4);
@@ -877,32 +865,31 @@
   bf16* hbT  = kb;
   if (off > ws_size) return;
 
-  wcast_k<<<1536, 256, 0, stream>>>(Wqkv, Wo, W1, W2, wqkvb, wob, w1b, w2b);
-  fuse_ln_k<<<576, 256, 0, stream>>>(img, gamma_f, beta_f, xnT);
-  mgemm_k<0><<<dim3(12, 288), 256, 0, stream>>>(wqkvb, xnT, nullptr, nullptr, nullptr,
+  mega0_k<<<2240, 256, 0, stream>>>(Wqkv, Wo, W1, W2, wqkvb, wob, w1b, w2b,
+      img, gamma_f, beta_f, xnT,
+      cls_embs, gamma_g, beta_g, Wg, gbuf, gnbb);
+  mgemm_k<0><<<3464, 256, 0, stream>>>(wqkvb, xnT, nullptr, nullptr, nullptr,
       nullptr, nullptr, nullptr, nullptr, nullptr, qssp, kssp,
-      qb, kb, vT, nullptr, nullptr, nullptr);
-  rownorm_red_k<<<4096, 64, 0, stream>>>(qssp, kssp, qn, kn);
-  clsg_k<<<NCLS, 256, 0, stream>>>(cls_embs, gamma_g, beta_g, Wg, gbuf, gnbb);
-  clsobj_k<<<8, 256, 0, stream>>>(gbuf, cls_logits, clsov);
-  gm1_k<<<dim3(32, GMBLK), 256, 0, stream>>>(qb, gnbb, gminp, gmaxp);
-  gmred_k<<<4096, 64, 0, stream>>>(gminp, gmaxp, gminv, gmsv);
-  seg_k<<<2048, 256, 0, stream>>>(seg, kb, segn);
-  segden_k<<<BB, 256, 0, stream>>>(seg, segd);
-  obj_k<<<1, 256, 0, stream>>>(clsov, segn, segd, objv);
-  aux_k<<<dim3(32, AUXBLK), 256, 0, stream>>>(kb, objv, auxv, apmin, apmax);
-  auxred_k<<<32, 64, 0, stream>>>(apmin, apmax, aminv, amsv);
-  attn_k<<<dim3(LSPLIT, 32), 256, 0, stream>>>(qb, kb, apart);
-  smax_k<<<32, 256, 0, stream>>>(apart, qn, kn, attn_scale, Pb);
+      qb, kb, vT, nullptr, nullptr, nullptr,
+      gbuf, cls_logits, clsov);
+  mega1_k<<<7940, 256, 0, stream>>>(qb, kb, gnbb, gminp, gmaxp, apart,
+      seg, segn, segd, qssp, kssp, qn, kn);
+  aux_k<<<dim3(32, AUXBLK), 256, 0, stream>>>(kb, clsov, segn, segd, auxv, apmin, apmax);
+  megared_k<<<1064, 256, 0, stream>>>(gminp, gmaxp, gminv, gmsv,
+      apmin, apmax, aminv, amsv,
+      apart, qn, kn, attn_scale, Pb);
   pv_k<<<dim3(32, GMBLK), 256, 0, stream>>>(qb, gnbb, auxv, gminv, gmsv, aminv, amsv, Pb, vT, outT);
   mgemm_k<1><<<dim3(4, 288), 256, 0, stream>>>(wob, outT, img, nullptr, bo,
       nullptr, nullptr, nullptr, nullptr, statp, nullptr, nullptr,
-      nullptr, nullptr, nullptr, xT, nullptr, nullptr);
-  statsred_k<<<BLPIX / 256, 256, 0, stream>>>(statp, mu1, rs1);
+      nullptr, nullptr, nullptr, xT, nullptr, nullptr,
+      nullptr, nullptr, nullptr);
+  statsred_k<<<144, 256, 0, stream>>>(statp, mu1, rs1);
   mgemm_k<2><<<dim3(4, 288), 256, 0, stream>>>(w1b, xT, nullptr, nullptr, b1,
       mu1, rs1, gamma_n, beta_n, nullptr, nullptr, nullptr,
-      nullptr, nullptr, nullptr, nullptr, nullptr, hbT);
+      nullptr, nullptr, nullptr, nullptr, nullptr, hbT,
+      nullptr, nullptr, nullptr);
   mgemm_k<3><<<dim3(4, 288), 256, 0, stream>>>(w2b, hbT, nullptr, xT, b2,
       nullptr, nullptr, nullptr, nullptr, nullptr, nullptr, nullptr,
-      nullptr, nullptr, nullptr, nullptr, outp, nullptr);
+      nullptr, nullptr, nullptr, nullptr, outp, nullptr,
+      nullptr, nullptr, nullptr);
 }
```
